# Optimization experiments

Hardware: AMD Instinct MI355X
Metric: run time of the kernel (lower is better)

## Reference

```python
import jax, jax.numpy as jnp
import numpy as np
from jax import lax

EPS = 1e-5
IC = 32  # inter_channels

def bn(x, g, b, m, v):
    sh = (1, -1, 1, 1)
    return (x - m.reshape(sh)) * (g.reshape(sh) * lax.rsqrt(v.reshape(sh) + EPS)) + b.reshape(sh)

def prelu(x, a):
    return jnp.where(x >= 0, x, a * x)

def conv1x1(x, w):  # x: [B,C,H,W], w: [O,C]
    return jnp.einsum('bchw,oc->bohw', x, w)

def dconv(x, w, d):  # 3x3 dilated conv, same padding
    return lax.conv_general_dilated(x, w, (1, 1), [(d, d), (d, d)], rhs_dilation=(d, d),
                                    dimension_numbers=('NCHW', 'OIHW', 'NCHW'))

def glca_forward(feature, q_w, q_gamma, q_beta, q_mean, q_var, q_alpha,
                 k_w, k_gamma, k_beta, k_mean, k_var, k_alpha,
                 v_w, v_gamma, v_beta, v_mean, v_var, v_alpha,
                 d1_w, d1_gamma, d1_beta, d1_mean, d1_var,
                 d2_w, d2_gamma, d2_beta, d2_mean, d2_var,
                 d3_w, d3_gamma, d3_beta, d3_mean, d3_var,
                 o_w, o_gamma, o_beta, o_mean, o_var, o_alpha):
    B, C, H, W = feature.shape
    q = prelu(bn(conv1x1(feature, q_w), q_gamma, q_beta, q_mean, q_var), q_alpha)  # [B,IC,H,W]
    k = prelu(bn(conv1x1(feature, k_w), k_gamma, k_beta, k_mean, k_var), k_alpha)
    val = prelu(bn(conv1x1(feature, v_w), v_gamma, v_beta, v_mean, v_var), v_alpha)
    qr = q.transpose(0, 3, 2, 1).reshape(B * W, H, IC)   # [BW,H,IC]
    kr = k.transpose(0, 3, 1, 2).reshape(B * W, IC, H)   # [BW,IC,H]
    att = jax.nn.softmax(jnp.matmul(qr, kr), axis=-1)    # [BW,H,H]
    branches = []
    for w, g, b, m, var, d in ((d1_w, d1_gamma, d1_beta, d1_mean, d1_var, 1),
                               (d2_w, d2_gamma, d2_beta, d2_mean, d2_var, 3),
                               (d3_w, d3_gamma, d3_beta, d3_mean, d3_var, 5)):
        t = jax.nn.relu(bn(dconv(val, w, d), g, b, m, var))          # [B,IC,H,W]
        # faithful to source: permute(0,3,1,2) then raw view to [BW,H,IC]
        t = t.transpose(0, 3, 1, 2).reshape(B * W, H, IC)
        branches.append(jnp.matmul(att, t))                          # [BW,H,IC]
    # faithful to source: cat along dim 0, then raw view(B,W,H,-1)
    res = jnp.concatenate(branches, axis=0).reshape(B, W, H, 3 * IC)
    res = res.transpose(0, 3, 2, 1)                                  # [B,3*IC,H,W]
    out = prelu(bn(conv1x1(res, o_w), o_gamma, o_beta, o_mean, o_var) + feature, o_alpha)
    return out

def setup_inputs() -> dict:
    B, C, H, W = 8, 256, 160, 160
    key = jax.random.key(0)
    ks = iter(jax.random.split(key, 48))
    d = {}
    d['feature'] = jax.random.normal(next(ks), (B, C, H, W), jnp.float32)
    for p in ('q', 'k', 'v'):
        d[p + '_w'] = jax.random.normal(next(ks), (IC, C), jnp.float32) * 0.05
        d[p + '_gamma'] = jax.random.uniform(next(ks), (IC,), jnp.float32, 0.5, 1.5)
        d[p + '_beta'] = jax.random.normal(next(ks), (IC,), jnp.float32) * 0.1
        d[p + '_mean'] = jax.random.normal(next(ks), (IC,), jnp.float32) * 0.1
        d[p + '_var'] = jax.random.uniform(next(ks), (IC,), jnp.float32, 0.5, 1.5)
        d[p + '_alpha'] = jnp.full((1,), 0.25, jnp.float32)
    for p in ('d1', 'd2', 'd3'):
        d[p + '_w'] = jax.random.normal(next(ks), (IC, IC, 3, 3), jnp.float32) * 0.05
        d[p + '_gamma'] = jax.random.uniform(next(ks), (IC,), jnp.float32, 0.5, 1.5)
        d[p + '_beta'] = jax.random.normal(next(ks), (IC,), jnp.float32) * 0.1
        d[p + '_mean'] = jax.random.normal(next(ks), (IC,), jnp.float32) * 0.1
        d[p + '_var'] = jax.random.uniform(next(ks), (IC,), jnp.float32, 0.5, 1.5)
    d['o_w'] = jax.random.normal(next(ks), (C, 3 * IC), jnp.float32) * 0.05
    d['o_gamma'] = jax.random.uniform(next(ks), (C,), jnp.float32, 0.5, 1.5)
    d['o_beta'] = jax.random.normal(next(ks), (C,), jnp.float32) * 0.1
    d['o_mean'] = jax.random.normal(next(ks), (C,), jnp.float32) * 0.1
    d['o_var'] = jax.random.uniform(next(ks), (C,), jnp.float32, 0.5, 1.5)
    d['o_alpha'] = jnp.full((1,), 0.25, jnp.float32)
    return d

def reference(feature, q_w, q_gamma, q_beta, q_mean, q_var, q_alpha,
              k_w, k_gamma, k_beta, k_mean, k_var, k_alpha,
              v_w, v_gamma, v_beta, v_mean, v_var, v_alpha,
              d1_w, d1_gamma, d1_beta, d1_mean, d1_var,
              d2_w, d2_gamma, d2_beta, d2_mean, d2_var,
              d3_w, d3_gamma, d3_beta, d3_mean, d3_var,
              o_w, o_gamma, o_beta, o_mean, o_var, o_alpha):
    return glca_forward(feature, q_w, q_gamma, q_beta, q_mean, q_var, q_alpha,
                        k_w, k_gamma, k_beta, k_mean, k_var, k_alpha,
                        v_w, v_gamma, v_beta, v_mean, v_var, v_alpha,
                        d1_w, d1_gamma, d1_beta, d1_mean, d1_var,
                        d2_w, d2_gamma, d2_beta, d2_mean, d2_var,
                        d3_w, d3_gamma, d3_beta, d3_mean, d3_var,
                        o_w, o_gamma, o_beta, o_mean, o_var, o_alpha)
```

## Files before the change

kernel.cpp:

```cpp
#include <hip/hip_runtime.h>

constexpr int Hh = 160, Ww = 160, Bb = 8, Cc = 256, ICn = 32;
constexpr int HWn = Hh * Ww;
constexpr float EPSf = 1e-5f;

constexpr int P_WQH  = 0;
constexpr int P_WQL  = 12288;
constexpr int P_QKVB = 24576;
constexpr int P_QKVA = 24672;
constexpr int P_DWB  = 24768;
constexpr int P_DB   = 52416;
constexpr int P_OWB  = 52512;
constexpr int P_OB   = 77088;
constexpr int P_OA   = 77344;
constexpr int PLANE  = Bb * ICn * HWn;
constexpr int OFF_Q  = 77824;
constexpr int OFF_K  = OFF_Q + PLANE;
constexpr int OFF_V  = OFF_Q + 2 * PLANE;
constexpr int OFF_T  = OFF_Q + 3 * PLANE;
constexpr int OFF_TPF= OFF_T + (3 * PLANE) / 2;
constexpr int OFF_CAT= OFF_Q + 6 * PLANE;

typedef unsigned short u16;
typedef short bf16x8 __attribute__((ext_vector_type(8)));
typedef float f32x4  __attribute__((ext_vector_type(4)));

__device__ __forceinline__ unsigned f2b(float x) {
    unsigned u = __float_as_uint(x);
    return (u + 0x7FFFu + ((u >> 16) & 1u)) >> 16;
}
__device__ __forceinline__ float b2f(unsigned b) { return __uint_as_float(b << 16); }

#define GLOAD_LDS16(gp, lp) __builtin_amdgcn_global_load_lds( \
    (const __attribute__((address_space(1))) void*)(gp), \
    (__attribute__((address_space(3))) void*)(lp), 16, 0, 0)

struct InPtrs { const float* p[40]; };

__global__ void k_prep(InPtrs in, float* __restrict__ ws) {
    int idx = blockIdx.x * 256 + threadIdx.x;
    if (idx < 24576) {
        int oc = idx >> 8, c = idx & 255;
        int z = oc >> 5, o = oc & 31;
        const float* wz = in.p[1 + 6 * z];
        float s = in.p[2 + 6 * z][o] * rsqrtf(in.p[5 + 6 * z][o] + EPSf);
        float wf = wz[o * 256 + c] * s;
        unsigned hi = f2b(wf);
        unsigned lo = f2b(wf - b2f(hi));
        ((u16*)(ws + P_WQH))[oc * 256 + c] = (u16)hi;
        ((u16*)(ws + P_WQL))[oc * 256 + c] = (u16)lo;
    } else if (idx < 24672) {
        int oc = idx - 24576; int z = oc >> 5, o = oc & 31;
        float s = in.p[2 + 6 * z][o] * rsqrtf(in.p[5 + 6 * z][o] + EPSf);
        ws[P_QKVB + oc] = in.p[3 + 6 * z][o] - in.p[4 + 6 * z][o] * s;
    } else if (idx < 24768) {
        int oc = idx - 24672; int z = oc >> 5;
        ws[P_QKVA + oc] = in.p[6 + 6 * z][0];
    } else if (idx < 52416) {
        int j = idx - 24768;
        int d = j / 9216, r2 = j % 9216;
        int oc = r2 & 31; int tmp = r2 >> 5;
        int kx = tmp % 3; tmp /= 3; int ky = tmp % 3; int ic2 = tmp / 3;
        const float* wd = in.p[19 + 5 * d];
        float s = in.p[20 + 5 * d][oc] * rsqrtf(in.p[23 + 5 * d][oc] + EPSf);
        float wf = wd[((oc * 32 + ic2) * 3 + ky) * 3 + kx] * s;
        ((u16*)(ws + P_DWB))[((d * 9 + ky * 3 + kx) * 32 + oc) * 32 + ic2] = (u16)f2b(wf);
    } else if (idx < 52512) {
        int j = idx - 52416; int d = j >> 5, oc = j & 31;
        float s = in.p[20 + 5 * d][oc] * rsqrtf(in.p[23 + 5 * d][oc] + EPSf);
        ws[P_DB + j] = in.p[21 + 5 * d][oc] - in.p[22 + 5 * d][oc] * s;
    } else if (idx < 77088) {
        int j2 = idx - 52512; int c = j2 / 96;
        float s = in.p[35][c] * rsqrtf(in.p[38][c] + EPSf);
        ((u16*)(ws + P_OWB))[j2] = (u16)f2b(in.p[34][j2] * s);
    } else if (idx < 77344) {
        int c = idx - 77088;
        float s = in.p[35][c] * rsqrtf(in.p[38][c] + EPSf);
        ws[P_OB + c] = in.p[36][c] - in.p[37][c] * s;
    } else if (idx == 77344) {
        ws[P_OA] = in.p[39][0];
    }
}

__global__ __launch_bounds__(64) void k_vpad(float* __restrict__ ws) {
    u16* Vt = (u16*)(ws + OFF_V);
    size_t base = (size_t)blockIdx.x * 176 * 32;
    int t = threadIdx.x;
    int off = (t < 32) ? t * 8 : (168 * 32 + (t - 32) * 8);
    uint4 z = {0u, 0u, 0u, 0u};
    *(uint4*)(Vt + base + off) = z;
}

__global__ __launch_bounds__(256) void k_qkv(const float* __restrict__ feat,
                                             float* __restrict__ ws) {
    extern __shared__ float FS[];
    const int tid = threadIdx.x;
    const int wv = tid >> 6, l = tid & 63;
    const int g = l >> 4, c15 = l & 15;
    const int n0 = blockIdx.x * 256;
    const int b = n0 / HWn, hw0 = n0 % HWn;
    const float* fbase = feat + (size_t)b * Cc * HWn + hw0;
    const u16* __restrict__ WQH = (const u16*)(ws + P_WQH);
    const u16* __restrict__ WQL = (const u16*)(ws + P_WQL);

    f32x4 acc[6][4];
    f32x4 z4 = {0.f, 0.f, 0.f, 0.f};
#pragma unroll
    for (int mt = 0; mt < 6; mt++)
#pragma unroll
        for (int i = 0; i < 4; i++) acc[mt][i] = z4;

#pragma unroll
    for (int j = 0; j < 8; j++) {
        int r = wv * 8 + j;
        GLOAD_LDS16(fbase + (size_t)r * HWn + l * 4, &FS[r * 256]);
    }
    __syncthreads();

    for (int kc = 0; kc < 8; kc++) {
        if (kc < 7) {
            float* dst = &FS[((kc + 1) & 1) * 8192];
#pragma unroll
            for (int j = 0; j < 8; j++) {
                int r = wv * 8 + j;
                GLOAD_LDS16(fbase + (size_t)((kc + 1) * 32 + r) * HWn + l * 4, dst + r * 256);
            }
        }
        const float* B = &FS[(kc & 1) * 8192];
        bf16x8 bh[4], bl[4];
#pragma unroll
        for (int i = 0; i < 4; i++) {
            const float* bp = B + (g * 8) * 256 + (wv * 4 + i) * 16 + c15;
            unsigned hw_[4], lw_[4];
#pragma unroll
            for (int v2 = 0; v2 < 4; v2++) {
                float x0 = bp[(2 * v2) * 256];
                float x1 = bp[(2 * v2 + 1) * 256];
                unsigned h0 = f2b(x0), h1 = f2b(x1);
                unsigned l0 = f2b(x0 - b2f(h0)), l1 = f2b(x1 - b2f(h1));
                hw_[v2] = h0 | (h1 << 16);
                lw_[v2] = l0 | (l1 << 16);
            }
            uint4 hv = {hw_[0], hw_[1], hw_[2], hw_[3]};
            uint4 lv = {lw_[0], lw_[1], lw_[2], lw_[3]};
            bh[i] = *(bf16x8*)&hv;
            bl[i] = *(bf16x8*)&lv;
        }
#pragma unroll
        for (int mt = 0; mt < 6; mt++) {
            int arow = (16 * mt + c15) * 256 + kc * 32 + g * 8;
            bf16x8 ah = *(const bf16x8*)(WQH + arow);
            bf16x8 al = *(const bf16x8*)(WQL + arow);
#pragma unroll
            for (int i = 0; i < 4; i++) {
                acc[mt][i] = __builtin_amdgcn_mfma_f32_16x16x32_bf16(ah, bh[i], acc[mt][i], 0, 0, 0);
                acc[mt][i] = __builtin_amdgcn_mfma_f32_16x16x32_bf16(ah, bl[i], acc[mt][i], 0, 0, 0);
                acc[mt][i] = __builtin_amdgcn_mfma_f32_16x16x32_bf16(al, bh[i], acc[mt][i], 0, 0, 0);
            }
        }
        __syncthreads();
    }

    u16* vt = (u16*)(ws + OFF_V);
#pragma unroll
    for (int mt = 0; mt < 6; mt++)
#pragma unroll
        for (int i = 0; i < 4; i++) {
            int pos = hw0 + (wv * 4 + i) * 16 + c15;
            if (mt < 4) {
#pragma unroll
                for (int jr = 0; jr < 4; jr++) {
                    int oc = 16 * mt + 4 * g + jr;
                    float bb = ws[P_QKVB + oc];
                    float aa = ws[P_QKVA + oc];
                    float y = acc[mt][i][jr] + bb;
                    y = y >= 0.f ? y : aa * y;
                    int z = oc >> 5, o = oc & 31;
                    ws[OFF_Q + (size_t)z * PLANE + ((size_t)b * ICn + o) * HWn + pos] = y;
                }
            } else {
                int h = pos / 160, w2 = pos % 160;
                unsigned r[2];
#pragma unroll
                for (int p = 0; p < 2; p++) {
                    int oc = 16 * mt + 4 * g + 2 * p;
                    float y0 = acc[mt][i][2 * p]     + ws[P_QKVB + oc];
                    float y1 = acc[mt][i][2 * p + 1] + ws[P_QKVB + oc + 1];
                    float a0 = ws[P_QKVA + oc], a1 = ws[P_QKVA + oc + 1];
                    y0 = y0 >= 0.f ? y0 : a0 * y0;
                    y1 = y1 >= 0.f ? y1 : a1 * y1;
                    r[p] = f2b(y0) | (f2b(y1) << 16);
                }
                size_t a = ((size_t)(b * 160 + h) * 176 + w2 + 8) * 32 + (mt - 4) * 16 + 4 * g;
                uint2 dd; dd.x = r[0]; dd.y = r[1];
                *(uint2*)(vt + a) = dd;
            }
        }
}

__global__ __launch_bounds__(256) void k_dconv(float* __restrict__ ws) {
    const int tid = threadIdx.x;
    const int wv = tid >> 6, l = tid & 63;
    const int g = l >> 4, c15 = l & 15;
    const int b = blockIdx.y;
    const int d = blockIdx.z;
    const int dil = 1 + 2 * d;
    const int h0 = blockIdx.x * 2;
    const u16* __restrict__ WB = (const u16*)(ws + P_DWB) + d * 9 * 32 * 32;
    bf16x8 wb[9][2];
#pragma unroll
    for (int tap = 0; tap < 9; tap++)
#pragma unroll
        for (int n = 0; n < 2; n++)
            wb[tap][n] = *(const bf16x8*)(WB + ((size_t)tap * 32 + n * 16 + c15) * 32 + g * 8);
    const u16* __restrict__ Vt = (const u16*)(ws + OFF_V) + (size_t)b * 160 * 176 * 32;
    const float bias0 = ws[P_DB + d * 32 + c15];
    const float bias1 = ws[P_DB + d * 32 + 16 + c15];
    u16* __restrict__ tp = (u16*)(ws + OFF_TPF) + (size_t)(d * Bb + b) * ICn * HWn;
    f32x4 z4 = {0.f, 0.f, 0.f, 0.f};

    for (int t5 = 0; t5 < 5; t5++) {
        int t = wv * 5 + t5;
        int h = h0 + (t >= 10);
        int w0 = (t % 10) * 16;
        f32x4 acc0 = z4, acc1 = z4;
#pragma unroll
        for (int ky = 0; ky < 3; ky++) {
            int hh = h + dil * (ky - 1);
            if ((unsigned)hh >= 160u) continue;
            const u16* row = Vt + (size_t)hh * 176 * 32;
#pragma unroll
            for (int kx = 0; kx < 3; kx++) {
                int wbase = w0 + dil * (kx - 1) + 8;
                bf16x8 av = *(const bf16x8*)(row + (size_t)(wbase + c15) * 32 + g * 8);
                acc0 = __builtin_amdgcn_mfma_f32_16x16x32_bf16(av, wb[ky * 3 + kx][0], acc0, 0, 0, 0);
                acc1 = __builtin_amdgcn_mfma_f32_16x16x32_bf16(av, wb[ky * 3 + kx][1], acc1, 0, 0, 0);
            }
        }
        size_t pixb = (size_t)h * 160 + w0 + 4 * g;
        uint2 o0, o1;
        o0.x = f2b(fmaxf(acc0[0] + bias0, 0.f)) | (f2b(fmaxf(acc0[1] + bias0, 0.f)) << 16);
        o0.y = f2b(fmaxf(acc0[2] + bias0, 0.f)) | (f2b(fmaxf(acc0[3] + bias0, 0.f)) << 16);
        o1.x = f2b(fmaxf(acc1[0] + bias1, 0.f)) | (f2b(fmaxf(acc1[1] + bias1, 0.f)) << 16);
        o1.y = f2b(fmaxf(acc1[2] + bias1, 0.f)) | (f2b(fmaxf(acc1[3] + bias1, 0.f)) << 16);
        *(uint2*)(tp + (size_t)c15 * HWn + pixb) = o0;
        *(uint2*)(tp + (size_t)(16 + c15) * HWn + pixb) = o1;
    }
}

__global__ __launch_bounds__(256) void k_tfrag(float* __restrict__ ws) {
    __shared__ u16 fr[4][5120];
    const int tid = threadIdx.x;
    const int wq = blockIdx.x;
    const int b  = blockIdx.y;
    const int d  = blockIdx.z;
    const int w0 = wq * 4;
    const u16* __restrict__ tp = (const u16*)(ws + OFF_TPF) + (size_t)(d * Bb + b) * ICn * HWn;
    for (int i = tid; i < 5120; i += 256) {
        int ic = i / 160, h = i % 160;
        uint2 v = *(const uint2*)(tp + (size_t)ic * HWn + h * Ww + w0);
        fr[0][i] = (u16)(v.x & 0xFFFFu);
        fr[1][i] = (u16)(v.x >> 16);
        fr[2][i] = (u16)(v.y & 0xFFFFu);
        fr[3][i] = (u16)(v.y >> 16);
    }
    __syncthreads();
    u16* __restrict__ tf = (u16*)(ws + OFF_T);
#pragma unroll
    for (int it = 0; it < 10; it++) {
        int W = tid + it * 256;
        int s = W / 640, word = W % 640;
        int slot = word >> 6, lane = word & 63;
        int jc = (lane & 15) | ((slot / 5) << 4);
        int h2b = ((slot % 5) << 5) | (((lane >> 4) & 3) << 3);
        unsigned r[4];
#pragma unroll
        for (int p = 0; p < 4; p++) {
            int f0 = (h2b + 2 * p) * 32 + jc;
            unsigned lo = fr[s][f0];
            unsigned hi = fr[s][f0 + 32];
            r[p] = lo | (hi << 16);
        }
        uint4 o4 = {r[0], r[1], r[2], r[3]};
        *(uint4*)(tf + ((size_t)d * 1280 + b * 160 + w0 + s) * 5120 + word * 8) = o4;
    }
}

__device__ __forceinline__ void stage_qk_hilo(const float* __restrict__ g,
                                              char* hi_buf, char* lo_buf, int tid) {
#pragma unroll
    for (int ss = 0; ss < 2; ss++) {
        int s = tid + ss * 320;
        int l = s & 63, rt = s >> 6;
        int h = 16 * rt + (l & 15);
        int icb = (l >> 4) * 8;
        const float* gp = g + (size_t)icb * HWn + h * Ww;
        unsigned hb[8], lb[8];
#pragma unroll
        for (int v = 0; v < 8; v++) {
            float x = gp[(size_t)v * HWn];
            hb[v] = f2b(x);
            lb[v] = f2b(x - b2f(hb[v]));
        }
        uint4 hv = {hb[0] | (hb[1] << 16), hb[2] | (hb[3] << 16),
                    hb[4] | (hb[5] << 16), hb[6] | (hb[7] << 16)};
        uint4 lv = {lb[0] | (lb[1] << 16), lb[2] | (lb[3] << 16),
                    lb[4] | (lb[5] << 16), lb[6] | (lb[7] << 16)};
        *(uint4*)(hi_buf + s * 16) = hv;
        *(uint4*)(lo_buf + s * 16) = lv;
    }
}

__global__ __launch_bounds__(320) void k_att(float* __restrict__ ws) {
    extern __shared__ char smem[];
    char* q_hi = smem;
    char* q_lo = smem + 10240;
    char* k_hi = smem + 20480;
    char* k_lo = smem + 30720;
    char* Sb   = smem;
    const int tid = threadIdx.x;
    const int bid = blockIdx.x;
    const int r8 = bid & 7, qq = bid >> 3;
    const int b = qq / 20;
    const int w = r8 * 20 + (qq % 20);
    const int bw = b * Ww + w;
    const int wv = tid >> 6;
    const int l  = tid & 63;
    const int g  = l >> 4;
    const int c  = l & 15;

    const float* qg = ws + OFF_Q + (size_t)b * ICn * HWn + w;
    const float* kg = ws + OFF_K + (size_t)b * ICn * HWn + w;
    stage_qk_hilo(qg, q_hi, q_lo, tid);
    stage_qk_hilo(kg, k_hi, k_lo, tid);
    __syncthreads();

    bf16x8 bq[2][2];
#pragma unroll
    for (int ct = 0; ct < 2; ct++) {
        int tau = 2 * wv + ct;
        bq[ct][0] = *(bf16x8*)(q_hi + (tau * 64 + l) * 16);
        bq[ct][1] = *(bf16x8*)(q_lo + (tau * 64 + l) * 16);
    }
    f32x4 acc[10][2];
    f32x4 z4 = {0.f, 0.f, 0.f, 0.f};
#pragma unroll
    for (int rt = 0; rt < 10; rt++) { acc[rt][0] = z4; acc[rt][1] = z4; }
#pragma unroll
    for (int rt = 0; rt < 10; rt++) {
        bf16x8 ah = *(bf16x8*)(k_hi + (rt * 64 + l) * 16);
        bf16x8 al = *(bf16x8*)(k_lo + (rt * 64 + l) * 16);
#pragma unroll
        for (int ct = 0; ct < 2; ct++) {
            acc[rt][ct] = __builtin_amdgcn_mfma_f32_16x16x32_bf16(ah, bq[ct][0], acc[rt][ct], 0, 0, 0);
            acc[rt][ct] = __builtin_amdgcn_mfma_f32_16x16x32_bf16(ah, bq[ct][1], acc[rt][ct], 0, 0, 0);
            acc[rt][ct] = __builtin_amdgcn_mfma_f32_16x16x32_bf16(al, bq[ct][0], acc[rt][ct], 0, 0, 0);
        }
    }
    __syncthreads();

    float mx[2] = {-3.4e38f, -3.4e38f};
#pragma unroll
    for (int rt = 0; rt < 10; rt++)
#pragma unroll
        for (int ct = 0; ct < 2; ct++)
#pragma unroll
            for (int j = 0; j < 4; j++) mx[ct] = fmaxf(mx[ct], acc[rt][ct][j]);
#pragma unroll
    for (int ct = 0; ct < 2; ct++) {
        mx[ct] = fmaxf(mx[ct], __shfl_xor(mx[ct], 16));
        mx[ct] = fmaxf(mx[ct], __shfl_xor(mx[ct], 32));
    }
    float sm[2] = {0.f, 0.f};
#pragma unroll
    for (int rt = 0; rt < 10; rt++)
#pragma unroll
        for (int ct = 0; ct < 2; ct++)
#pragma unroll
            for (int j = 0; j < 4; j++) {
                float e = __expf(acc[rt][ct][j] - mx[ct]);
                acc[rt][ct][j] = e;
                sm[ct] += e;
            }
#pragma unroll
    for (int ct = 0; ct < 2; ct++) {
        sm[ct] += __shfl_xor(sm[ct], 16);
        sm[ct] += __shfl_xor(sm[ct], 32);
    }
    float inv[2] = {1.f / sm[0], 1.f / sm[1]};

#pragma unroll
    for (int rt = 0; rt < 10; rt++) {
#pragma unroll
        for (int ct = 0; ct < 2; ct++) {
            float p0 = acc[rt][ct][0] * inv[ct];
            float p1 = acc[rt][ct][1] * inv[ct];
            float p2 = acc[rt][ct][2] * inv[ct];
            float p3 = acc[rt][ct][3] * inv[ct];
            unsigned d0 = f2b(p0) | (f2b(p1) << 16);
            unsigned d1 = f2b(p2) | (f2b(p3) << 16);
            int Lf = c + 16 * (2 * (rt & 1) + (g >> 1));
            char* dst = Sb + (((wv * 2 + ct) * 5 + (rt >> 1)) * 64 + Lf) * 16 + 8 * (g & 1);
            uint2 dd; dd.x = d0; dd.y = d1;
            *(uint2*)dst = dd;
        }
    }
    __syncthreads();

    const u16* tf = (const u16*)(ws + OFF_T);
    u16* catb = (u16*)(ws + OFF_CAT);
    for (int d = 0; d < 3; d++) {
        const u16* tfd = tf + ((size_t)d * (Bb * Ww) + bw) * 5120;
        f32x4 po[2][2];
        po[0][0] = z4; po[0][1] = z4; po[1][0] = z4; po[1][1] = z4;
#pragma unroll
        for (int ks = 0; ks < 5; ks++) {
            bf16x8 a0 = *(const bf16x8*)(tfd + ((0 * 5 + ks) * 64 + l) * 8);
            bf16x8 a1 = *(const bf16x8*)(tfd + ((1 * 5 + ks) * 64 + l) * 8);
            bf16x8 s0 = *(bf16x8*)(Sb + (((wv * 2 + 0) * 5 + ks) * 64 + l) * 16);
            bf16x8 s1 = *(bf16x8*)(Sb + (((wv * 2 + 1) * 5 + ks) * 64 + l) * 16);
            po[0][0] = __builtin_amdgcn_mfma_f32_16x16x32_bf16(a0, s0, po[0][0], 0, 0, 0);
            po[0][1] = __builtin_amdgcn_mfma_f32_16x16x32_bf16(a0, s1, po[0][1], 0, 0, 0);
            po[1][0] = __builtin_amdgcn_mfma_f32_16x16x32_bf16(a1, s0, po[1][0], 0, 0, 0);
            po[1][1] = __builtin_amdgcn_mfma_f32_16x16x32_bf16(a1, s1, po[1][1], 0, 0, 0);
        }
#pragma unroll
        for (int jt = 0; jt < 2; jt++)
#pragma unroll
            for (int ct = 0; ct < 2; ct++) {
                int h1 = 32 * wv + 16 * ct + c;
                size_t idx = (size_t)d * PLANE + (size_t)bw * 5120 + h1 * 32 + 16 * jt + 4 * g;
                f32x4 v = po[jt][ct];
                uint2 dd;
                dd.x = f2b(v[0]) | (f2b(v[1]) << 16);
                dd.y = f2b(v[2]) | (f2b(v[3]) << 16);
                *(uint2*)(catb + idx) = dd;
            }
    }
}

__global__ __launch_bounds__(256) void k_out(const float* __restrict__ feat,
                                             const float* __restrict__ ws,
                                             float* __restrict__ out) {
    __shared__ u16 Bs[12288];
    const int tid = threadIdx.x;
    const int wv = tid >> 6, l = tid & 63;
    const int g = l >> 4, c15 = l & 15;
    const int n0 = blockIdx.x * 128;
    const int b = n0 / HWn, hw0 = n0 % HWn;
    const u16* __restrict__ CATb = (const u16*)(ws + OFF_CAT);
    const u16* __restrict__ OWB = (const u16*)(ws + P_OWB);

#pragma unroll
    for (int ss = 0; ss < 6; ss++) {
        int s = tid + ss * 256;
        int sl = s & 63, si = s >> 6;
        int p = (si & 7) * 16 + (sl & 15);
        int hw = hw0 + p;
        int h = hw / Ww, w2 = hw % Ww;
        int j = (si >> 3) * 32 + (sl >> 4) * 8;
        size_t flat = ((size_t)(b * Ww + w2) * Hh + h) * 96 + j;
        *(uint4*)(&Bs[(si * 64 + sl) * 8]) = *(const uint4*)(CATb + flat);
    }
    bf16x8 af[4][3];
#pragma unroll
    for (int mt = 0; mt < 4; mt++)
#pragma unroll
        for (int ks = 0; ks < 3; ks++)
            af[mt][ks] = *(const bf16x8*)(OWB + (wv * 64 + mt * 16 + c15) * 96 + ks * 32 + g * 8);
    __syncthreads();
    const float alpha = ws[P_OA];

    f32x4 z4 = {0.f, 0.f, 0.f, 0.f};
#pragma unroll
    for (int np = 0; np < 2; np++) {
        f32x4 acc[4][4];
#pragma unroll
        for (int mt = 0; mt < 4; mt++)
#pragma unroll
            for (int ntl = 0; ntl < 4; ntl++) acc[mt][ntl] = z4;
#pragma unroll
        for (int ks = 0; ks < 3; ks++) {
            bf16x8 bf_[4];
#pragma unroll
            for (int ntl = 0; ntl < 4; ntl++)
                bf_[ntl] = *(const bf16x8*)(&Bs[((ks * 8 + np * 4 + ntl) * 64 + l) * 8]);
#pragma unroll
            for (int mt = 0; mt < 4; mt++)
#pragma unroll
                for (int ntl = 0; ntl < 4; ntl++)
                    acc[mt][ntl] = __builtin_amdgcn_mfma_f32_16x16x32_bf16(af[mt][ks], bf_[ntl], acc[mt][ntl], 0, 0, 0);
        }
#pragma unroll
        for (int mt = 0; mt < 4; mt++)
#pragma unroll
            for (int ntl = 0; ntl < 4; ntl++) {
                int p = (np * 4 + ntl) * 16 + c15;
#pragma unroll
                for (int jr = 0; jr < 4; jr++) {
                    int cch = wv * 64 + mt * 16 + 4 * g + jr;
                    size_t base = ((size_t)b * Cc + cch) * HWn + hw0 + p;
                    float y = acc[mt][ntl][jr] + ws[P_OB + cch] + feat[base];
                    out[base] = y >= 0.f ? y : alpha * y;
                }
            }
    }
}

extern "C" void kernel_launch(void* const* d_in, const int* in_sizes, int n_in,
                              void* d_out, int out_size, void* d_ws, size_t ws_size,
                              hipStream_t stream) {
    InPtrs ip;
    for (int i = 0; i < 40; i++) ip.p[i] = (const float*)d_in[i];
    float* ws = (float*)d_ws;
    const float* feat = (const float*)d_in[0];
    float* out = (float*)d_out;

    k_prep<<<304, 256, 0, stream>>>(ip, ws);
    k_vpad<<<1280, 64, 0, stream>>>(ws);
    (void)hipFuncSetAttribute(reinterpret_cast<const void*>(k_qkv),
                              hipFuncAttributeMaxDynamicSharedMemorySize, 65536);
    k_qkv<<<800, 256, 65536, stream>>>(feat, ws);
    k_dconv<<<dim3(80, 8, 3), 256, 0, stream>>>(ws);
    k_tfrag<<<dim3(40, 8, 3), 256, 0, stream>>>(ws);
    (void)hipFuncSetAttribute(reinterpret_cast<const void*>(k_att),
                              hipFuncAttributeMaxDynamicSharedMemorySize, 51200);
    k_att<<<1280, 320, 51200, stream>>>(ws);
    k_out<<<1600, 256, 0, stream>>>(feat, ws, out);
}
```

Measured before the change: 459.5 us.

## Shrink QKV projection tile to 64 pixels and load all channels upfront

The QKV 1x1-conv kernel now handles 64 pixels per block instead of 256. All 256 input channels for those pixels are loaded into shared memory in one pass, replacing the double-buffered channel-chunk pipeline, and the grid grows fourfold to 3200 blocks. This gives more blocks for occupancy and load balance and fewer accumulator registers per thread. The cost is that each block re-reads the weight fragments per pixel tile, loses load/compute overlap within a block, and writes outputs in narrower contiguous runs.

```diff
diff --git a/kernel.cpp b/kernel.cpp
--- a/kernel.cpp
+++ b/kernel.cpp
@@ -97,105 +97,85 @@
     const int tid = threadIdx.x;
     const int wv = tid >> 6, l = tid & 63;
     const int g = l >> 4, c15 = l & 15;
-    const int n0 = blockIdx.x * 256;
+    const int n0 = blockIdx.x * 64;
     const int b = n0 / HWn, hw0 = n0 % HWn;
     const float* fbase = feat + (size_t)b * Cc * HWn + hw0;
     const u16* __restrict__ WQH = (const u16*)(ws + P_WQH);
     const u16* __restrict__ WQL = (const u16*)(ws + P_WQL);
 
-    f32x4 acc[6][4];
+#pragma unroll
+    for (int j = 0; j < 16; j++) {
+        int r4 = (wv * 16 + j) * 4;
+        GLOAD_LDS16(fbase + (size_t)(r4 + (l >> 4)) * HWn + (l & 15) * 4, &FS[r4 * 64]);
+    }
+    __syncthreads();
+
+    f32x4 acc[6];
     f32x4 z4 = {0.f, 0.f, 0.f, 0.f};
 #pragma unroll
-    for (int mt = 0; mt < 6; mt++)
-#pragma unroll
-        for (int i = 0; i < 4; i++) acc[mt][i] = z4;
-
-#pragma unroll
-    for (int j = 0; j < 8; j++) {
-        int r = wv * 8 + j;
-        GLOAD_LDS16(fbase + (size_t)r * HWn + l * 4, &FS[r * 256]);
-    }
-    __syncthreads();
-
+    for (int mt = 0; mt < 6; mt++) acc[mt] = z4;
+
+#pragma unroll
     for (int kc = 0; kc < 8; kc++) {
-        if (kc < 7) {
-            float* dst = &FS[((kc + 1) & 1) * 8192];
-#pragma unroll
-            for (int j = 0; j < 8; j++) {
-                int r = wv * 8 + j;
-                GLOAD_LDS16(fbase + (size_t)((kc + 1) * 32 + r) * HWn + l * 4, dst + r * 256);
-            }
-        }
-        const float* B = &FS[(kc & 1) * 8192];
-        bf16x8 bh[4], bl[4];
-#pragma unroll
-        for (int i = 0; i < 4; i++) {
-            const float* bp = B + (g * 8) * 256 + (wv * 4 + i) * 16 + c15;
-            unsigned hw_[4], lw_[4];
-#pragma unroll
-            for (int v2 = 0; v2 < 4; v2++) {
-                float x0 = bp[(2 * v2) * 256];
-                float x1 = bp[(2 * v2 + 1) * 256];
-                unsigned h0 = f2b(x0), h1 = f2b(x1);
-                unsigned l0 = f2b(x0 - b2f(h0)), l1 = f2b(x1 - b2f(h1));
-                hw_[v2] = h0 | (h1 << 16);
-                lw_[v2] = l0 | (l1 << 16);
-            }
-            uint4 hv = {hw_[0], hw_[1], hw_[2], hw_[3]};
-            uint4 lv = {lw_[0], lw_[1], lw_[2], lw_[3]};
-            bh[i] = *(bf16x8*)&hv;
-            bl[i] = *(bf16x8*)&lv;
-        }
+        const float* bp = FS + (size_t)(kc * 32 + g * 8) * 64 + wv * 16 + c15;
+        unsigned hw_[4], lw_[4];
+#pragma unroll
+        for (int v2 = 0; v2 < 4; v2++) {
+            float x0 = bp[(2 * v2) * 64];
+            float x1 = bp[(2 * v2 + 1) * 64];
+            unsigned h0 = f2b(x0), h1 = f2b(x1);
+            unsigned l0 = f2b(x0 - b2f(h0)), l1 = f2b(x1 - b2f(h1));
+            hw_[v2] = h0 | (h1 << 16);
+            lw_[v2] = l0 | (l1 << 16);
+        }
+        uint4 hv = {hw_[0], hw_[1], hw_[2], hw_[3]};
+        uint4 lv = {lw_[0], lw_[1], lw_[2], lw_[3]};
+        bf16x8 bh = *(bf16x8*)&hv;
+        bf16x8 bl = *(bf16x8*)&lv;
 #pragma unroll
         for (int mt = 0; mt < 6; mt++) {
             int arow = (16 * mt + c15) * 256 + kc * 32 + g * 8;
             bf16x8 ah = *(const bf16x8*)(WQH + arow);
             bf16x8 al = *(const bf16x8*)(WQL + arow);
-#pragma unroll
-            for (int i = 0; i < 4; i++) {
-                acc[mt][i] = __builtin_amdgcn_mfma_f32_16x16x32_bf16(ah, bh[i], acc[mt][i], 0, 0, 0);
-                acc[mt][i] = __builtin_amdgcn_mfma_f32_16x16x32_bf16(ah, bl[i], acc[mt][i], 0, 0, 0);
-                acc[mt][i] = __builtin_amdgcn_mfma_f32_16x16x32_bf16(al, bh[i], acc[mt][i], 0, 0, 0);
+            acc[mt] = __builtin_amdgcn_mfma_f32_16x16x32_bf16(ah, bh, acc[mt], 0, 0, 0);
+            acc[mt] = __builtin_amdgcn_mfma_f32_16x16x32_bf16(ah, bl, acc[mt], 0, 0, 0);
+            acc[mt] = __builtin_amdgcn_mfma_f32_16x16x32_bf16(al, bh, acc[mt], 0, 0, 0);
+        }
+    }
+
+    u16* vt = (u16*)(ws + OFF_V);
+    const int pos = hw0 + wv * 16 + c15;
+#pragma unroll
+    for (int mt = 0; mt < 6; mt++) {
+        if (mt < 4) {
+#pragma unroll
+            for (int jr = 0; jr < 4; jr++) {
+                int oc = 16 * mt + 4 * g + jr;
+                float bb = ws[P_QKVB + oc];
+                float aa = ws[P_QKVA + oc];
+                float y = acc[mt][jr] + bb;
+                y = y >= 0.f ? y : aa * y;
+                int z = oc >> 5, o = oc & 31;
+                ws[OFF_Q + (size_t)z * PLANE + ((size_t)b * ICn + o) * HWn + pos] = y;
             }
-        }
-        __syncthreads();
-    }
-
-    u16* vt = (u16*)(ws + OFF_V);
-#pragma unroll
-    for (int mt = 0; mt < 6; mt++)
-#pragma unroll
-        for (int i = 0; i < 4; i++) {
-            int pos = hw0 + (wv * 4 + i) * 16 + c15;
-            if (mt < 4) {
-#pragma unroll
-                for (int jr = 0; jr < 4; jr++) {
-                    int oc = 16 * mt + 4 * g + jr;
-                    float bb = ws[P_QKVB + oc];
-                    float aa = ws[P_QKVA + oc];
-                    float y = acc[mt][i][jr] + bb;
-                    y = y >= 0.f ? y : aa * y;
-                    int z = oc >> 5, o = oc & 31;
-                    ws[OFF_Q + (size_t)z * PLANE + ((size_t)b * ICn + o) * HWn + pos] = y;
-                }
-            } else {
-                int h = pos / 160, w2 = pos % 160;
-                unsigned r[2];
-#pragma unroll
-                for (int p = 0; p < 2; p++) {
-                    int oc = 16 * mt + 4 * g + 2 * p;
-                    float y0 = acc[mt][i][2 * p]     + ws[P_QKVB + oc];
-                    float y1 = acc[mt][i][2 * p + 1] + ws[P_QKVB + oc + 1];
-                    float a0 = ws[P_QKVA + oc], a1 = ws[P_QKVA + oc + 1];
-                    y0 = y0 >= 0.f ? y0 : a0 * y0;
-                    y1 = y1 >= 0.f ? y1 : a1 * y1;
-                    r[p] = f2b(y0) | (f2b(y1) << 16);
-                }
-                size_t a = ((size_t)(b * 160 + h) * 176 + w2 + 8) * 32 + (mt - 4) * 16 + 4 * g;
-                uint2 dd; dd.x = r[0]; dd.y = r[1];
-                *(uint2*)(vt + a) = dd;
+        } else {
+            int h = pos / 160, w2 = pos % 160;
+            unsigned r[2];
+#pragma unroll
+            for (int p = 0; p < 2; p++) {
+                int oc = 16 * mt + 4 * g + 2 * p;
+                float y0 = acc[mt][2 * p]     + ws[P_QKVB + oc];
+                float y1 = acc[mt][2 * p + 1] + ws[P_QKVB + oc + 1];
+                float a0 = ws[P_QKVA + oc], a1 = ws[P_QKVA + oc + 1];
+                y0 = y0 >= 0.f ? y0 : a0 * y0;
+                y1 = y1 >= 0.f ? y1 : a1 * y1;
+                r[p] = f2b(y0) | (f2b(y1) << 16);
             }
-        }
+            size_t a = ((size_t)(b * 160 + h) * 176 + w2 + 8) * 32 + (mt - 4) * 16 + 4 * g;
+            uint2 dd; dd.x = r[0]; dd.y = r[1];
+            *(uint2*)(vt + a) = dd;
+        }
+    }
 }
 
 __global__ __launch_bounds__(256) void k_dconv(float* __restrict__ ws) {
@@ -520,7 +500,7 @@
     k_vpad<<<1280, 64, 0, stream>>>(ws);
     (void)hipFuncSetAttribute(reinterpret_cast<const void*>(k_qkv),
                               hipFuncAttributeMaxDynamicSharedMemorySize, 65536);
-    k_qkv<<<800, 256, 65536, stream>>>(feat, ws);
+    k_qkv<<<3200, 256, 65536, stream>>>(feat, ws);
     k_dconv<<<dim3(80, 8, 3), 256, 0, stream>>>(ws);
     k_tfrag<<<dim3(40, 8, 3), 256, 0, stream>>>(ws);
     (void)hipFuncSetAttribute(reinterpret_cast<const void*>(k_att),
```

After: 535.4 us. 16.5% more time.
